# Kernel optimization log

Measured on AMD Instinct MI355X. Metric: run time of the kernel, lower is better.

Reference implementation:

```python
import jax, jax.numpy as jnp
import numpy as np
from jax import lax

B, S, V, E, H, T = 128, 512, 30000, 256, 256, 9
PAD_ID = 0


def setup_inputs() -> dict:
    key = jax.random.key(0)
    ks = jax.random.split(key, 16)
    u = lambda k, sh, s: jax.random.uniform(k, sh, jnp.float32, -s, s)
    sc = 1.0 / float(np.sqrt(H))
    so = 1.0 / float(np.sqrt(2 * H))
    input_ids = jax.random.randint(ks[0], (B, S), 1, V)
    lengths = jax.random.randint(ks[1], (B,), 1, S + 1)
    mask = jnp.arange(S)[None, :] < lengths[:, None]  # left-contiguous valid mask
    embed_table = jax.random.normal(ks[2], (V, E), jnp.float32).at[PAD_ID].set(0.0)
    return dict(
        input_ids=input_ids,
        mask=mask,
        embed_table=embed_table,
        W_ih_f=u(ks[3], (4 * H, E), sc), W_hh_f=u(ks[4], (4 * H, H), sc), b_f=u(ks[5], (4 * H,), sc),
        W_ih_b=u(ks[6], (4 * H, E), sc), W_hh_b=u(ks[7], (4 * H, H), sc), b_b=u(ks[8], (4 * H,), sc),
        W_out=u(ks[9], (T, 2 * H), so), b_out=u(ks[10], (T,), so),
        start_trans=u(ks[11], (T,), 0.1), end_trans=u(ks[12], (T,), 0.1), trans=u(ks[13], (T, T), 0.1),
    )


def _lstm_dir(xg, W_hh, reverse):
    # xg: [S, B, 4H] precomputed input projection + bias; torch gate order i,f,g,o
    def step(carry, g_in):
        h, c = carry
        g = g_in + h @ W_hh.T
        i, f, gg, o = jnp.split(g, 4, axis=-1)
        c = jax.nn.sigmoid(f) * c + jax.nn.sigmoid(i) * jnp.tanh(gg)
        h = jax.nn.sigmoid(o) * jnp.tanh(c)
        return (h, c), h
    b, hdim = xg.shape[1], W_hh.shape[1]
    init = (jnp.zeros((b, hdim), xg.dtype), jnp.zeros((b, hdim), xg.dtype))
    _, hs = lax.scan(step, init, xg, reverse=reverse)
    return hs  # [S, B, H]


def _emissions(input_ids, embed_table, W_ih_f, W_hh_f, b_f, W_ih_b, W_hh_b, b_b, W_out, b_out):
    x = embed_table[input_ids]                                  # [B, S, E]
    xg_f = jnp.einsum('bse,ge->sbg', x, W_ih_f) + b_f           # [S, B, 4H]
    xg_b = jnp.einsum('bse,ge->sbg', x, W_ih_b) + b_b
    h_f = _lstm_dir(xg_f, W_hh_f, reverse=False)
    h_b = _lstm_dir(xg_b, W_hh_b, reverse=True)
    h = jnp.concatenate([h_f, h_b], axis=-1)                    # [S, B, 2H]
    return jnp.einsum('sbh,th->sbt', h, W_out) + b_out          # [S, B, T]


def reference(input_ids, mask, embed_table, W_ih_f, W_hh_f, b_f, W_ih_b, W_hh_b, b_b,
              W_out, b_out, start_trans, end_trans, trans):
    em = _emissions(input_ids, embed_table, W_ih_f, W_hh_f, b_f, W_ih_b, W_hh_b, b_b, W_out, b_out)
    maskT = mask.T  # [S, B]

    # ---- Viterbi forward (torchcrf._viterbi_decode semantics) ----
    score0 = start_trans + em[0]  # [B, T]

    def vstep(score, inp):
        em_t, m_t = inp  # [B,T], [B]
        nxt = score[:, :, None] + trans[None, :, :] + em_t[:, None, :]  # [B, T, T]
        idx = jnp.argmax(nxt, axis=1)        # [B, T] backpointers
        best = jnp.max(nxt, axis=1)          # [B, T]
        score = jnp.where(m_t[:, None], best, score)
        return score, idx

    score, history = lax.scan(vstep, score0, (em[1:], maskT[1:]))  # history: [S-1, B, T]
    last_tag = jnp.argmax(score + end_trans, axis=-1)              # [B]

    # ---- Backtrace (mask-aware; frontier stays put on padded steps) ----
    def btstep(tag, inp):
        hist_t, m_t = inp  # [B,T], [B]
        out = tag
        prev = jnp.take_along_axis(hist_t, tag[:, None], axis=1)[:, 0]
        tag = jnp.where(m_t, prev, tag)
        return tag, out

    tag0, tags_rest = lax.scan(btstep, last_tag, (history, maskT[1:]), reverse=True)
    tags = jnp.concatenate([tag0[None, :], tags_rest], axis=0).T  # [B, S]
    return jnp.where(mask, tags, 0).astype(jnp.int32)
```

## Files before the change

kernel.cpp:

```cpp
#include <hip/hip_runtime.h>
#include <hip/hip_bf16.h>

#define SEQ   512
#define BATCH 128
#define VOCAB 30000
#define EDIM  256
#define HDIM  256
#define NT    9

__global__ void k_detect(const unsigned char* __restrict__ m, int* __restrict__ flag) {
    __shared__ int ok_sh;
    if (threadIdx.x == 0) ok_sh = 1;
    __syncthreads();
    int b = threadIdx.x;
    const uint4* row = (const uint4*)(m + b * SEQ);
    int ok = 1, prev = 1;
    for (int i = 0; i < SEQ / 16; ++i) {
        uint4 v = row[i];
        unsigned w[4] = {v.x, v.y, v.z, v.w};
        #pragma unroll
        for (int wi = 0; wi < 4; ++wi) {
            #pragma unroll
            for (int j = 0; j < 4; ++j) {
                int byte = (w[wi] >> (8 * j)) & 255;
                if (byte > 1 || byte > prev) ok = 0;
                prev = byte;
            }
        }
    }
    if (!ok) atomicAnd(&ok_sh, 0);
    __syncthreads();
    if (threadIdx.x == 0) *flag = ok_sh;
}

__global__ __launch_bounds__(256) void k_table_gemm(
    const float* __restrict__ emb, const float* __restrict__ Wf,
    const float* __restrict__ Wb, const float* __restrict__ bf,
    const float* __restrict__ bb, float* __restrict__ table) {
    __shared__ __align__(16) float As[64][68];
    __shared__ __align__(16) float Bs[64][68];
    int t  = threadIdx.x;
    int tx = t & 15, ty = t >> 4;
    int n0 = blockIdx.x * 64;
    int v0 = blockIdx.y * 64;
    float acc[4][4] = {};
    for (int kc = 0; kc < 4; ++kc) {
        #pragma unroll
        for (int rr = 0; rr < 4; ++rr) {
            int slot = t + rr * 256;
            int m = slot >> 4, kq = slot & 15;
            int v = v0 + m;
            float4 a = (v < VOCAB)
                ? *(const float4*)&emb[v * EDIM + kc * 64 + kq * 4]
                : make_float4(0.f, 0.f, 0.f, 0.f);
            As[kq * 4 + 0][m] = a.x; As[kq * 4 + 1][m] = a.y;
            As[kq * 4 + 2][m] = a.z; As[kq * 4 + 3][m] = a.w;
            int n = n0 + m;
            const float* Wrow = (n < 1024) ? &Wf[n * 256] : &Wb[(n - 1024) * 256];
            float4 bvec = *(const float4*)&Wrow[kc * 64 + kq * 4];
            Bs[kq * 4 + 0][m] = bvec.x; Bs[kq * 4 + 1][m] = bvec.y;
            Bs[kq * 4 + 2][m] = bvec.z; Bs[kq * 4 + 3][m] = bvec.w;
        }
        __syncthreads();
        #pragma unroll
        for (int k = 0; k < 64; ++k) {
            float4 a = *(const float4*)&As[k][ty * 4];
            float4 b = *(const float4*)&Bs[k][tx * 4];
            acc[0][0] += a.x * b.x; acc[0][1] += a.x * b.y; acc[0][2] += a.x * b.z; acc[0][3] += a.x * b.w;
            acc[1][0] += a.y * b.x; acc[1][1] += a.y * b.y; acc[1][2] += a.y * b.z; acc[1][3] += a.y * b.w;
            acc[2][0] += a.z * b.x; acc[2][1] += a.z * b.y; acc[2][2] += a.z * b.z; acc[2][3] += a.z * b.w;
            acc[3][0] += a.w * b.x; acc[3][1] += a.w * b.y; acc[3][2] += a.w * b.z; acc[3][3] += a.w * b.w;
        }
        __syncthreads();
    }
    int n = n0 + tx * 4;
    const float* bi = (n < 1024) ? &bf[n] : &bb[n - 1024];
    float4 bias = *(const float4*)bi;
    #pragma unroll
    for (int i = 0; i < 4; ++i) {
        int v = v0 + ty * 4 + i;
        if (v < VOCAB) {
            float4 o;
            o.x = acc[i][0] + bias.x; o.y = acc[i][1] + bias.y;
            o.z = acc[i][2] + bias.z; o.w = acc[i][3] + bias.w;
            *(float4*)&table[(size_t)v * 2048 + n] = o;
        }
    }
}

#define DPPXOR(dst, src, CTRL) { \
    int _i = __float_as_int(src); \
    int _r = __builtin_amdgcn_update_dpp(_i, _i, (CTRL), 0xF, 0xF, false); \
    dst = __int_as_float(_r); }

__global__ __attribute__((amdgpu_flat_work_group_size(512, 512), amdgpu_waves_per_eu(4, 4)))
void k_lstm_cl(
    const int* __restrict__ ids, const float* __restrict__ Whhf,
    const float* __restrict__ Whhb, const float* __restrict__ table,
    const float* __restrict__ Wout, float* __restrict__ emp,
    float* hx, int* tagbuf) {
    __shared__ float h_cur[4][256];
    __shared__ float h_em[256];
    __shared__ float sh_g[4][132];
    __shared__ float wout_s[NT][257];
    __shared__ int   sh_ctr;

    const int t   = threadIdx.x;
    const int bid = blockIdx.x;
    const int cluster = bid >> 3;
    const int myd = bid & 7;
    const int dir = cluster & 1;
    const int quad = cluster >> 1;
    const int gbatch = quad * 4 + myd;

    const int lane = t & 63;
    const int wv   = t >> 6;
    const int g    = t >> 4;
    const int kc   = t & 15;

    const int nb = (t >> 5) & 3;
    const int nd = t & 31;

    const int em = t - 256;
    const int etg = em >> 4, el = em & 15;

    const float* Whh = dir ? Whhb : Whhf;

    if (t == 0) sh_ctr = 0;
    for (int idx = t; idx < NT * 256; idx += 512)
        wout_s[idx >> 8][idx & 255] = Wout[(idx >> 8) * 512 + dir * 256 + (idx & 255)];
    for (int idx = t; idx < 1024; idx += 512)
        h_cur[idx >> 8][idx & 255] = 0.f;
    float c_state = 0.f;

    float4 w0_0, w0_1, w0_2, w0_3, w1_0, w1_1, w1_2, w1_3;
    float4 w2_0, w2_1, w2_2, w2_3, w3_0, w3_1, w3_2, w3_3;
    {
        int lr0 = 4 * g, lr1 = 4 * g + 1, lr2 = 4 * g + 2, lr3 = 4 * g + 3;
        int gr0 = (lr0 >> 5) * 256 + myd * 32 + (lr0 & 31);
        int gr1 = (lr1 >> 5) * 256 + myd * 32 + (lr1 & 31);
        int gr2 = (lr2 >> 5) * 256 + myd * 32 + (lr2 & 31);
        int gr3 = (lr3 >> 5) * 256 + myd * 32 + (lr3 & 31);
        const float4* wp0 = (const float4*)(Whh + (size_t)gr0 * 256);
        const float4* wp1 = (const float4*)(Whh + (size_t)gr1 * 256);
        const float4* wp2 = (const float4*)(Whh + (size_t)gr2 * 256);
        const float4* wp3 = (const float4*)(Whh + (size_t)gr3 * 256);
        w0_0 = wp0[kc]; w0_1 = wp0[kc + 16]; w0_2 = wp0[kc + 32]; w0_3 = wp0[kc + 48];
        w1_0 = wp1[kc]; w1_1 = wp1[kc + 16]; w1_2 = wp1[kc + 32]; w1_3 = wp1[kc + 48];
        w2_0 = wp2[kc]; w2_1 = wp2[kc + 16]; w2_2 = wp2[kc + 32]; w2_3 = wp2[kc + 48];
        w3_0 = wp3[kc]; w3_1 = wp3[kc + 16]; w3_2 = wp3[kc + 32]; w3_3 = wp3[kc + 48];
    }
    __syncthreads();

    float xi = 0.f, xf = 0.f, xq = 0.f, xo = 0.f;
    if (t < 128) {
        int s0 = dir ? SEQ - 1 : 0;
        int id = ids[(quad * 4 + nb) * SEQ + s0];
        const float* tb = table + (size_t)id * 2048 + dir * 1024;
        int base = myd * 32 + nd;
        xi = tb[base]; xf = tb[256 + base]; xq = tb[512 + base]; xo = tb[768 + base];
    }

    #pragma unroll 1
    for (int it = 0; it < SEQ; ++it) {
        if (myd < 4 && t < 256) h_em[t] = h_cur[myd][t];

        float a[16];
        #pragma unroll
        for (int m = 0; m < 16; ++m) a[m] = 0.f;

        #define DOTJ(J, W0, W1, W2, W3) { \
            const int off = 4 * (kc + 16 * (J)); \
            _Pragma("unroll") \
            for (int b = 0; b < 4; ++b) { \
                float4 hv = *(const float4*)(&h_cur[b][0] + off); \
                a[b]      += W0.x*hv.x + W0.y*hv.y + W0.z*hv.z + W0.w*hv.w; \
                a[4 + b]  += W1.x*hv.x + W1.y*hv.y + W1.z*hv.z + W1.w*hv.w; \
                a[8 + b]  += W2.x*hv.x + W2.y*hv.y + W2.z*hv.z + W2.w*hv.w; \
                a[12 + b] += W3.x*hv.x + W3.y*hv.y + W3.z*hv.z + W3.w*hv.w; } }
        DOTJ(0, w0_0, w1_0, w2_0, w3_0)
        DOTJ(1, w0_1, w1_1, w2_1, w3_1)
        DOTJ(2, w0_2, w1_2, w2_2, w3_2)
        DOTJ(3, w0_3, w1_3, w2_3, w3_3)
        #undef DOTJ

        #pragma unroll
        for (int m = 0; m < 8; ++m) {
            int bit = kc & 1;
            float sent = bit ? a[m] : a[m + 8];
            float recv; DPPXOR(recv, sent, 0xB1)
            a[m] = (bit ? a[m + 8] : a[m]) + recv;
        }
        #pragma unroll
        for (int m = 0; m < 4; ++m) {
            int bit = kc & 2;
            float sent = bit ? a[m] : a[m + 4];
            float recv; DPPXOR(recv, sent, 0x4E)
            a[m] = (bit ? a[m + 4] : a[m]) + recv;
        }
        #pragma unroll
        for (int m = 0; m < 2; ++m) {
            int bit = kc & 4;
            float sent = bit ? a[m] : a[m + 2];
            float recv = __shfl_xor(sent, 4);
            a[m] = (bit ? a[m + 2] : a[m]) + recv;
        }
        {
            int bit = kc & 8;
            float sent = bit ? a[0] : a[1];
            float recv; DPPXOR(recv, sent, 0x128)
            a[0] = (bit ? a[1] : a[0]) + recv;
        }
        {
            int tile = ((kc & 1) << 3) | ((kc & 2) << 1) | ((kc & 4) >> 1) | ((kc & 8) >> 3);
            sh_g[tile & 3][4 * g + (tile >> 2)] = a[0];
        }
        __syncthreads();

        const int p = it & 1;
        float* hxp = hx + (size_t)p * 65536 + (size_t)cluster * 1024;
        int* tags = tagbuf + p * 512 + cluster * 8;

        if (t < 128) {
            float iv = sh_g[nb][nd]      + xi;
            float fv = sh_g[nb][32 + nd] + xf;
            float gv = sh_g[nb][64 + nd] + xq;
            float ov = sh_g[nb][96 + nd] + xo;
            float si = 1.f / (1.f + expf(-iv));
            float sf = 1.f / (1.f + expf(-fv));
            float so = 1.f / (1.f + expf(-ov));
            float tg = tanhf(gv);
            c_state = sf * c_state + si * tg;
            float hh = so * tanhf(c_state);
            int dl = myd * 32 + nd;
            h_cur[nb][dl] = hh;
            __hip_atomic_store(&hxp[nb * 256 + dl], hh,
                               __ATOMIC_RELAXED, __HIP_MEMORY_SCOPE_AGENT);
            asm volatile("s_waitcnt vmcnt(0)" ::: "memory");
            if (lane == 0) atomicAdd(&sh_ctr, 1);
            if (t == 0) {
                while (__hip_atomic_load(&sh_ctr, __ATOMIC_RELAXED,
                                         __HIP_MEMORY_SCOPE_WORKGROUP) < 2 * (it + 1)) {}
                __hip_atomic_store(&tags[myd], it,
                                   __ATOMIC_RELAXED, __HIP_MEMORY_SCOPE_AGENT);
            }
            if (it < SEQ - 1) {
                int sn = dir ? (SEQ - 2 - it) : (it + 1);
                int id = ids[(quad * 4 + nb) * SEQ + sn];
                const float* tb = table + (size_t)id * 2048 + dir * 1024;
                int base = myd * 32 + nd;
                xi = tb[base]; xf = tb[256 + base]; xq = tb[512 + base]; xo = tb[768 + base];
            }
        } else if (em >= 0 && em < 144 && myd < 4) {
            if (it > 0) {
                int sp = dir ? (SEQ - it) : (it - 1);
                float pe = 0.f;
                #pragma unroll
                for (int j = 0; j < 16; ++j)
                    pe += wout_s[etg][el + 16 * j] * h_em[el + 16 * j];
                pe += __shfl_xor(pe, 1); pe += __shfl_xor(pe, 2);
                pe += __shfl_xor(pe, 4); pe += __shfl_xor(pe, 8);
                if (el == 0)
                    emp[(((size_t)(dir * BATCH) + gbatch) * SEQ + sp) * NT + etg] = pe;
            }
        }

        if (wv != myd) {
            while (__hip_atomic_load(&tags[wv], __ATOMIC_RELAXED,
                                     __HIP_MEMORY_SCOPE_AGENT) != it)
                __builtin_amdgcn_s_sleep(1);
            #pragma unroll
            for (int rep = 0; rep < 2; ++rep) {
                int idx = rep * 64 + lane;
                int b2 = idx >> 5, nd2 = idx & 31;
                float vv = __hip_atomic_load(&hxp[b2 * 256 + wv * 32 + nd2],
                                             __ATOMIC_RELAXED, __HIP_MEMORY_SCOPE_AGENT);
                h_cur[b2][wv * 32 + nd2] = vv;
            }
        }
        __syncthreads();
    }

    if (myd < 4 && t < 256) h_em[t] = h_cur[myd][t];
    __syncthreads();
    if (myd < 4 && t < 144) {
        int etg2 = t >> 4, el2 = t & 15;
        int sp = dir ? 0 : (SEQ - 1);
        float pe = 0.f;
        #pragma unroll
        for (int j = 0; j < 16; ++j)
            pe += wout_s[etg2][el2 + 16 * j] * h_em[el2 + 16 * j];
        pe += __shfl_xor(pe, 1); pe += __shfl_xor(pe, 2);
        pe += __shfl_xor(pe, 4); pe += __shfl_xor(pe, 8);
        if (el2 == 0)
            emp[(((size_t)(dir * BATCH) + gbatch) * SEQ + sp) * NT + etg2] = pe;
    }
}

__global__ __launch_bounds__(64) void k_viterbi(
    const float* __restrict__ emp, const float* __restrict__ b_out,
    const float* __restrict__ start_t, const float* __restrict__ end_t,
    const float* __restrict__ trans, const void* __restrict__ maskp,
    const int* __restrict__ mask_is_bool, int* __restrict__ out) {
    __shared__ float sh_em[SEQ][NT];
    __shared__ float sh_score[NT];
    __shared__ float sh_trans[NT * NT];
    __shared__ unsigned char sh_mask[SEQ];
    __shared__ unsigned char sh_hist[SEQ - 1][NT];
    __shared__ unsigned char sh_tags[SEQ];
    int b = blockIdx.x;
    int t = threadIdx.x;
    int isb = *mask_is_bool;
    for (int idx = t; idx < SEQ * NT; idx += 64) {
        int s = idx / NT, tg = idx % NT;
        sh_em[s][tg] = emp[((size_t)b * SEQ + s) * NT + tg]
                     + emp[(((size_t)BATCH + b) * SEQ + s) * NT + tg]
                     + b_out[tg];
    }
    if (isb) {
        const unsigned char* m8 = (const unsigned char*)maskp;
        for (int idx = t; idx < SEQ; idx += 64) sh_mask[idx] = m8[b * SEQ + idx];
    } else {
        const int* m32 = (const int*)maskp;
        for (int idx = t; idx < SEQ; idx += 64) sh_mask[idx] = (unsigned char)(m32[b * SEQ + idx] != 0);
    }
    for (int idx = t; idx < NT * NT; idx += 64) sh_trans[idx] = trans[idx];
    __syncthreads();
    float sc = 0.f;
    if (t < NT) { sc = start_t[t] + sh_em[0][t]; sh_score[t] = sc; }
    __syncthreads();
    for (int s = 1; s < SEQ; ++s) {
        if (t < NT) {
            float m = -3.4e38f; int bp = 0;
            #pragma unroll
            for (int i = 0; i < NT; ++i) {
                float v = sh_score[i] + sh_trans[i * NT + t];
                if (v > m) { m = v; bp = i; }
            }
            sh_hist[s - 1][t] = (unsigned char)bp;
            float best = m + sh_em[s][t];
            if (sh_mask[s]) sc = best;
        }
        __syncthreads();
        if (t < NT) sh_score[t] = sc;
        __syncthreads();
    }
    if (t == 0) {
        float bb = -3.4e38f; int tag = 0;
        for (int j = 0; j < NT; ++j) {
            float v = sh_score[j] + end_t[j];
            if (v > bb) { bb = v; tag = j; }
        }
        for (int pos = SEQ - 1; pos >= 1; --pos) {
            sh_tags[pos] = (unsigned char)tag;
            if (sh_mask[pos]) tag = sh_hist[pos - 1][tag];
        }
        sh_tags[0] = (unsigned char)tag;
    }
    __syncthreads();
    for (int idx = t; idx < SEQ; idx += 64) {
        out[b * SEQ + idx] = sh_mask[idx] ? (int)sh_tags[idx] : 0;
    }
}

extern "C" void kernel_launch(void* const* d_in, const int* in_sizes, int n_in,
                              void* d_out, int out_size, void* d_ws, size_t ws_size,
                              hipStream_t stream) {
    const int*   ids  = (const int*)d_in[0];
    const void*  mask = d_in[1];
    const float* emb  = (const float*)d_in[2];
    const float* Wihf = (const float*)d_in[3];
    const float* Whhf = (const float*)d_in[4];
    const float* bfv  = (const float*)d_in[5];
    const float* Wihb = (const float*)d_in[6];
    const float* Whhb = (const float*)d_in[7];
    const float* bbv  = (const float*)d_in[8];
    const float* Wout = (const float*)d_in[9];
    const float* bout = (const float*)d_in[10];
    const float* st   = (const float*)d_in[11];
    const float* en   = (const float*)d_in[12];
    const float* tr   = (const float*)d_in[13];
    int* out = (int*)d_out;

    char* ws = (char*)d_ws;
    float* table = (float*)ws;
    float* emp   = (float*)(ws + 245760000);
    float* hx    = (float*)(ws + 245760000 + 4718592);
    int*   tags  = (int*)(ws + 245760000 + 4718592 + 524288);
    int*   flag  = (int*)(ws + 245760000 + 4718592 + 524288 + 4096);

    k_detect<<<1, 128, 0, stream>>>((const unsigned char*)mask, flag);
    dim3 g1(32, 469);
    k_table_gemm<<<g1, 256, 0, stream>>>(emb, Wihf, Wihb, bfv, bbv, table);
    k_lstm_cl<<<512, 512, 0, stream>>>(ids, Whhf, Whhb, table, Wout, emp, hx, tags);
    k_viterbi<<<128, 64, 0, stream>>>(emp, bout, st, en, tr, mask, flag, out);
}
```

Measured before the change: 3.422 ms.

## Replace per-step block barrier with triple-buffered h and per-chunk LDS flags

Removes the end-of-step __syncthreads in the LSTM recurrence. The hidden state is triple-buffered, and per-wave LDS flags with acquire/release ordering signal when each 32-column chunk of h is ready. Each dot-product chunk starts as soon as its slice arrives, so compute overlaps with the cross-block exchange. The emission projection moves onto the local wave that no longer copies remote data. The cost is more spin-waiting and more complex memory ordering, with some risk of races if the flags are wrong.

Measured after the change: 5.000 ms. 1.46x slower.

```diff
diff --git a/kernel.cpp b/kernel.cpp
--- a/kernel.cpp
+++ b/kernel.cpp
@@ -99,10 +99,11 @@
     const float* __restrict__ Whhb, const float* __restrict__ table,
     const float* __restrict__ Wout, float* __restrict__ emp,
     float* hx, int* tagbuf) {
-    __shared__ float h_cur[4][256];
-    __shared__ float h_em[256];
+    __shared__ float h_cur[3][4][256];
     __shared__ float sh_g[4][132];
-    __shared__ float wout_s[NT][257];
+    __shared__ float wout_s[NT][260];
+    __shared__ int   sh_flag[8];
+    __shared__ int   sh_flagN[2];
     __shared__ int   sh_ctr;
 
     const int t   = threadIdx.x;
@@ -121,16 +122,15 @@
     const int nb = (t >> 5) & 3;
     const int nd = t & 31;
 
-    const int em = t - 256;
-    const int etg = em >> 4, el = em & 15;
-
     const float* Whh = dir ? Whhb : Whhf;
 
     if (t == 0) sh_ctr = 0;
+    if (t < 8) sh_flag[t] = -1;
+    if (t < 2) sh_flagN[t] = -1;
     for (int idx = t; idx < NT * 256; idx += 512)
         wout_s[idx >> 8][idx & 255] = Wout[(idx >> 8) * 512 + dir * 256 + (idx & 255)];
     for (int idx = t; idx < 1024; idx += 512)
-        h_cur[idx >> 8][idx & 255] = 0.f;
+        h_cur[0][idx >> 8][idx & 255] = 0.f;
     float c_state = 0.f;
 
     float4 w0_0, w0_1, w0_2, w0_3, w1_0, w1_1, w1_2, w1_3;
@@ -161,28 +161,41 @@
         xi = tb[base]; xf = tb[256 + base]; xq = tb[512 + base]; xo = tb[768 + base];
     }
 
+    int b0 = 0, bw = 1, be = 2;
+
     #pragma unroll 1
     for (int it = 0; it < SEQ; ++it) {
-        if (myd < 4 && t < 256) h_em[t] = h_cur[myd][t];
+        const int tgt = it - 1;
+        #define SPINC(c) { \
+            if ((c) == myd) { \
+                while (__hip_atomic_load(&sh_flagN[0], __ATOMIC_ACQUIRE, __HIP_MEMORY_SCOPE_WORKGROUP) < tgt || \
+                       __hip_atomic_load(&sh_flagN[1], __ATOMIC_ACQUIRE, __HIP_MEMORY_SCOPE_WORKGROUP) < tgt) \
+                    __builtin_amdgcn_s_sleep(1); \
+            } else { \
+                while (__hip_atomic_load(&sh_flag[c], __ATOMIC_ACQUIRE, __HIP_MEMORY_SCOPE_WORKGROUP) < tgt) \
+                    __builtin_amdgcn_s_sleep(1); } }
 
         float a[16];
         #pragma unroll
         for (int m = 0; m < 16; ++m) a[m] = 0.f;
+        const float* hb = &h_cur[b0][0][0];
 
         #define DOTJ(J, W0, W1, W2, W3) { \
             const int off = 4 * (kc + 16 * (J)); \
             _Pragma("unroll") \
             for (int b = 0; b < 4; ++b) { \
-                float4 hv = *(const float4*)(&h_cur[b][0] + off); \
+                float4 hv = *(const float4*)(hb + b * 256 + off); \
                 a[b]      += W0.x*hv.x + W0.y*hv.y + W0.z*hv.z + W0.w*hv.w; \
                 a[4 + b]  += W1.x*hv.x + W1.y*hv.y + W1.z*hv.z + W1.w*hv.w; \
                 a[8 + b]  += W2.x*hv.x + W2.y*hv.y + W2.z*hv.z + W2.w*hv.w; \
                 a[12 + b] += W3.x*hv.x + W3.y*hv.y + W3.z*hv.z + W3.w*hv.w; } }
-        DOTJ(0, w0_0, w1_0, w2_0, w3_0)
-        DOTJ(1, w0_1, w1_1, w2_1, w3_1)
-        DOTJ(2, w0_2, w1_2, w2_2, w3_2)
-        DOTJ(3, w0_3, w1_3, w2_3, w3_3)
+
+        SPINC(0) SPINC(1) DOTJ(0, w0_0, w1_0, w2_0, w3_0)
+        SPINC(2) SPINC(3) DOTJ(1, w0_1, w1_1, w2_1, w3_1)
+        SPINC(4) SPINC(5) DOTJ(2, w0_2, w1_2, w2_2, w3_2)
+        SPINC(6) SPINC(7) DOTJ(3, w0_3, w1_3, w2_3, w3_3)
         #undef DOTJ
+        #undef SPINC
 
         #pragma unroll
         for (int m = 0; m < 8; ++m) {
@@ -233,7 +246,9 @@
             c_state = sf * c_state + si * tg;
             float hh = so * tanhf(c_state);
             int dl = myd * 32 + nd;
-            h_cur[nb][dl] = hh;
+            h_cur[bw][nb][dl] = hh;
+            if (lane == 0)
+                __hip_atomic_store(&sh_flagN[wv], it, __ATOMIC_RELEASE, __HIP_MEMORY_SCOPE_WORKGROUP);
             __hip_atomic_store(&hxp[nb * 256 + dl], hh,
                                __ATOMIC_RELAXED, __HIP_MEMORY_SCOPE_AGENT);
             asm volatile("s_waitcnt vmcnt(0)" ::: "memory");
@@ -250,18 +265,6 @@
                 const float* tb = table + (size_t)id * 2048 + dir * 1024;
                 int base = myd * 32 + nd;
                 xi = tb[base]; xf = tb[256 + base]; xq = tb[512 + base]; xo = tb[768 + base];
-            }
-        } else if (em >= 0 && em < 144 && myd < 4) {
-            if (it > 0) {
-                int sp = dir ? (SEQ - it) : (it - 1);
-                float pe = 0.f;
-                #pragma unroll
-                for (int j = 0; j < 16; ++j)
-                    pe += wout_s[etg][el + 16 * j] * h_em[el + 16 * j];
-                pe += __shfl_xor(pe, 1); pe += __shfl_xor(pe, 2);
-                pe += __shfl_xor(pe, 4); pe += __shfl_xor(pe, 8);
-                if (el == 0)
-                    emp[(((size_t)(dir * BATCH) + gbatch) * SEQ + sp) * NT + etg] = pe;
             }
         }
 
@@ -275,21 +278,50 @@
                 int b2 = idx >> 5, nd2 = idx & 31;
                 float vv = __hip_atomic_load(&hxp[b2 * 256 + wv * 32 + nd2],
                                              __ATOMIC_RELAXED, __HIP_MEMORY_SCOPE_AGENT);
-                h_cur[b2][wv * 32 + nd2] = vv;
-            }
-        }
-        __syncthreads();
-    }
-
-    if (myd < 4 && t < 256) h_em[t] = h_cur[myd][t];
+                h_cur[bw][b2][wv * 32 + nd2] = vv;
+            }
+            if (lane == 0)
+                __hip_atomic_store(&sh_flag[wv], it, __ATOMIC_RELEASE, __HIP_MEMORY_SCOPE_WORKGROUP);
+        } else if (myd < 4 && it > 0) {
+            int sp = dir ? (SEQ - it) : (it - 1);
+            int eg = lane >> 3, ee = lane & 7;
+            const float* hsrc = &h_cur[b0][myd][0];
+            float pe = 0.f;
+            #pragma unroll
+            for (int j = 0; j < 8; ++j) {
+                float4 h4 = *(const float4*)(hsrc + ee * 32 + j * 4);
+                float4 w4 = *(const float4*)(&wout_s[eg][ee * 32 + j * 4]);
+                pe += h4.x*w4.x + h4.y*w4.y + h4.z*w4.z + h4.w*w4.w;
+            }
+            pe += __shfl_xor(pe, 1); pe += __shfl_xor(pe, 2); pe += __shfl_xor(pe, 4);
+            if (ee == 0)
+                emp[(((size_t)(dir * BATCH) + gbatch) * SEQ + sp) * NT + eg] = pe;
+            if (eg == 0) {
+                float p8 = 0.f;
+                #pragma unroll
+                for (int j = 0; j < 8; ++j) {
+                    float4 h4 = *(const float4*)(hsrc + ee * 32 + j * 4);
+                    float4 w4 = *(const float4*)(&wout_s[8][ee * 32 + j * 4]);
+                    p8 += h4.x*w4.x + h4.y*w4.y + h4.z*w4.z + h4.w*w4.w;
+                }
+                p8 += __shfl_xor(p8, 1); p8 += __shfl_xor(p8, 2); p8 += __shfl_xor(p8, 4);
+                if (ee == 0)
+                    emp[(((size_t)(dir * BATCH) + gbatch) * SEQ + sp) * NT + 8] = p8;
+            }
+        }
+
+        int btmp = b0; b0 = bw; bw = be; be = btmp;
+    }
+
     __syncthreads();
     if (myd < 4 && t < 144) {
+        const int bfin = SEQ % 3;
         int etg2 = t >> 4, el2 = t & 15;
         int sp = dir ? 0 : (SEQ - 1);
         float pe = 0.f;
         #pragma unroll
         for (int j = 0; j < 16; ++j)
-            pe += wout_s[etg2][el2 + 16 * j] * h_em[el2 + 16 * j];
+            pe += wout_s[etg2][el2 + 16 * j] * h_cur[bfin][myd][el2 + 16 * j];
         pe += __shfl_xor(pe, 1); pe += __shfl_xor(pe, 2);
         pe += __shfl_xor(pe, 4); pe += __shfl_xor(pe, 8);
         if (el2 == 0)
```
